# Optimization experiments

Measured on AMD Instinct MI355X. Metric: run time of the kernel, lower is better.

## Reference

```python
import jax, jax.numpy as jnp
import numpy as np

WINDOW = 4  # window_size
H = 8       # n_heads


def setup_inputs() -> dict:
    key = jax.random.key(0)
    ks = jax.random.split(key, 12)
    B, C, T = 4, 512, 1024
    d = C // H
    x = jax.random.normal(ks[0], (B, C, T), dtype=jnp.float32)
    mask = jnp.ones((B, 1, 1, T), dtype=jnp.int32)
    s = 0.02
    Wq = jax.random.normal(ks[1], (C, C), dtype=jnp.float32) * s
    Wk = jax.random.normal(ks[2], (C, C), dtype=jnp.float32) * s
    Wv = jax.random.normal(ks[3], (C, C), dtype=jnp.float32) * s
    Wo = jax.random.normal(ks[4], (C, C), dtype=jnp.float32) * s
    bq = jnp.zeros((C,), jnp.float32)
    bk = jnp.zeros((C,), jnp.float32)
    bv = jnp.zeros((C,), jnp.float32)
    bo = jnp.zeros((C,), jnp.float32)
    rel_std = d ** (-0.5)
    emb_rel_k = jax.random.normal(ks[5], (1, 2 * WINDOW + 1, d), dtype=jnp.float32) * rel_std
    emb_rel_v = jax.random.normal(ks[6], (1, 2 * WINDOW + 1, d), dtype=jnp.float32) * rel_std
    return {"x": x, "mask": mask, "Wq": Wq, "bq": bq, "Wk": Wk, "bk": bk,
            "Wv": Wv, "bv": bv, "Wo": Wo, "bo": bo,
            "emb_rel_k": emb_rel_k, "emb_rel_v": emb_rel_v}


def _slice_rel_emb(emb, T, pad_len, start, end):
    # F.pad(emb, [0,0,pad,pad,0,0]) then [:, start:end] -> [1, 2T-1, d]
    p = jnp.pad(emb, ((0, 0), (pad_len, pad_len), (0, 0)))
    return p[:, start:end]


def reference(x, mask, Wq, bq, Wk, bk, Wv, bv, Wo, bo, emb_rel_k, emb_rel_v):
    B, C, T = x.shape
    d = C // H
    scale = jnp.asarray(np.sqrt(d), x.dtype)

    def proj(Wm, bm):
        return jnp.einsum('oc,bct->bot', Wm, x) + bm[None, :, None]

    def to_heads(t):  # [B,C,T] -> [B,H,T,d]
        return t.reshape(B, H, d, T).transpose(0, 1, 3, 2)

    query = to_heads(proj(Wq, bq))
    key_ = to_heads(proj(Wk, bk))
    value = to_heads(proj(Wv, bv))

    score = jnp.einsum('bhtd,bhsd->bhts', query, key_) / scale

    pad_len = max(0, T - (WINDOW + 1))
    start = max(0, WINDOW + 1 - T)
    end = start + 2 * T - 1

    k_emb = _slice_rel_emb(emb_rel_k, T, pad_len, start, end)  # [1, 2T-1, d]
    rel = jnp.einsum('bhtd,rd->bhtr', query, k_emb[0])          # [B,H,T,2T-1]
    # skew trick: relative -> absolute
    rel = jnp.pad(rel, ((0, 0), (0, 0), (0, 0), (0, 1))).reshape(B, H, 2 * T * T)
    rel = jnp.pad(rel, ((0, 0), (0, 0), (0, T - 1))).reshape(B, H, T + 1, 2 * T - 1)
    score_loc = rel[:, :, :T, T - 1:] / scale
    score = score + score_loc

    score = jnp.where(mask == 0, jnp.asarray(-10000.0, score.dtype), score)
    p_attn = jax.nn.softmax(score, axis=-1)  # dropout=0 (eval)

    output = jnp.einsum('bhts,bhsd->bhtd', p_attn, value)

    # inverse skew: absolute -> relative weights [B,H,T,2T-1]
    pw = jnp.pad(p_attn, ((0, 0), (0, 0), (0, 0), (0, T - 1))).reshape(B, H, T * (2 * T - 1))
    pw = jnp.pad(pw, ((0, 0), (0, 0), (T, 0))).reshape(B, H, T, 2 * T)[:, :, :, 1:]
    v_emb = _slice_rel_emb(emb_rel_v, T, pad_len, start, end)  # [1, 2T-1, d]
    output = output + jnp.einsum('bhtr,rd->bhtd', pw, v_emb[0])

    out = output.transpose(0, 1, 3, 2).reshape(B, C, T)
    return jnp.einsum('oc,bct->bot', Wo, out) + bo[None, :, None]
```

## Files before the change

kernel.cpp:

```cpp
#include <hip/hip_runtime.h>

typedef unsigned short u16;
typedef unsigned int u32;
using f32x4 = __attribute__((ext_vector_type(4))) float;
using s16x8 = __attribute__((ext_vector_type(8))) short;
using u16x4 = __attribute__((ext_vector_type(4))) unsigned short;
using u16x8 = __attribute__((ext_vector_type(8))) unsigned short;

namespace {

constexpr int T = 1024;
constexpr int C = 512;

__device__ inline u16 f2bf(float f) {
  u32 u = __builtin_bit_cast(u32, f);
  u32 r = (u + 0x7fffu + ((u >> 16) & 1u)) >> 16;
  return (u16)r;
}
__device__ inline float bf2f(u16 v) {
  return __builtin_bit_cast(float, (u32)v << 16);
}
__device__ inline f32x4 mfma16(s16x8 a, s16x8 b, f32x4 c) {
  return __builtin_amdgcn_mfma_f32_16x16x32_bf16(a, b, c, 0, 0, 0);
}

__global__ __launch_bounds__(256) void convert_all(
    const float* __restrict__ x, const float* __restrict__ Wq,
    const float* __restrict__ Wk, const float* __restrict__ Wv,
    const float* __restrict__ Wo, u16* __restrict__ xb, u16* __restrict__ Wqb,
    u16* __restrict__ Wkb, u16* __restrict__ Wvb, u16* __restrict__ Wob) {
  const int tid = threadIdx.x;
  const int bid = blockIdx.x;
  const float* src;
  u16* dst;
  size_t off;
  if (bid < 2048) {
    src = x; dst = xb;
    off = ((size_t)bid * 256 + tid) * 4;
  } else {
    const int j = bid - 2048;
    const int w = j >> 8;
    src = w == 0 ? Wq : w == 1 ? Wk : w == 2 ? Wv : Wo;
    dst = w == 0 ? Wqb : w == 1 ? Wkb : w == 2 ? Wvb : Wob;
    off = (((size_t)(j & 255)) * 256 + tid) * 4;
  }
  const float4 v = *reinterpret_cast<const float4*>(src + off);
  u16x4 o;
  o[0] = f2bf(v.x); o[1] = f2bf(v.y); o[2] = f2bf(v.z); o[3] = f2bf(v.w);
  *reinterpret_cast<u16x4*>(dst + off) = o;
}

__global__ __launch_bounds__(256) void qkv_gemm(
    const u16* __restrict__ xb, const u16* __restrict__ Wqb,
    const u16* __restrict__ Wkb, const u16* __restrict__ Wvb,
    const float* __restrict__ bq, const float* __restrict__ bk,
    const float* __restrict__ bv, u16* __restrict__ qb, u16* __restrict__ kb,
    u16* __restrict__ vb) {
  __shared__ u16 Bs[2][128 * 32];
  __shared__ float sbias[64];
  const int tid = threadIdx.x;
  const int z = blockIdx.z;
  const int b = z / 3, wsel = z - 3 * b;
  const u16* W = wsel == 0 ? Wqb : wsel == 1 ? Wkb : Wvb;
  const float* bias = wsel == 0 ? bq : wsel == 1 ? bk : bv;
  const int o0 = blockIdx.y * 64;
  const int t0 = blockIdx.x * 128;
  if (tid < 16)
    *reinterpret_cast<float4*>(&sbias[tid * 4]) =
        *reinterpret_cast<const float4*>(&bias[o0 + tid * 4]);

  const int l = tid & 63, wid = tid >> 6;
  const int wm = wid >> 1, wn = wid & 1;
  const int lr = l & 15, lg = l >> 4;

  const int cpair = tid & 15, tgrp = tid >> 4;
  const u16* xrow =
      xb + ((size_t)(b * C) + 2 * cpair) * T + t0 + 8 * tgrp;

  const u16* Arow0 = W + (size_t)(o0 + 32 * wm + lr) * C + 8 * lg;
  const u16* Arow1 = Arow0 + 16 * C;

  f32x4 acc[2][4] = {};

  auto stage = [&](int kk, int buf) {
    const u16* p = xrow + (size_t)kk * 32 * T;
    const u16x8 v0 = *reinterpret_cast<const u16x8*>(p);
    const u16x8 v1 = *reinterpret_cast<const u16x8*>(p + T);
    char* base = (char*)&Bs[buf][0];
#pragma unroll
    for (int j = 0; j < 8; ++j) {
      const int t = 8 * tgrp + j;
      const u32 w2 = (u32)v0[j] | ((u32)v1[j] << 16);
      *(u32*)(base + ((t * 64 + 4 * cpair) ^ ((t & 3) << 4))) = w2;
    }
  };

  s16x8 a0 = *reinterpret_cast<const s16x8*>(Arow0);
  s16x8 a1 = *reinterpret_cast<const s16x8*>(Arow1);
  stage(0, 0);
  __syncthreads();

  for (int kk = 0; kk < 16; ++kk) {
    s16x8 an0, an1;
    if (kk < 15) {
      an0 = *reinterpret_cast<const s16x8*>(Arow0 + (kk + 1) * 32);
      an1 = *reinterpret_cast<const s16x8*>(Arow1 + (kk + 1) * 32);
      stage(kk + 1, (kk + 1) & 1);
    }
    const char* rb = (const char*)&Bs[kk & 1][0];
#pragma unroll
    for (int nf = 0; nf < 4; ++nf) {
      const int t = 64 * wn + 16 * nf + lr;
      const s16x8 bfrag = *reinterpret_cast<const s16x8*>(
          rb + ((t * 64 + 16 * lg) ^ ((t & 3) << 4)));
      acc[0][nf] = mfma16(a0, bfrag, acc[0][nf]);
      acc[1][nf] = mfma16(a1, bfrag, acc[1][nf]);
    }
    __syncthreads();
    if (kk < 15) { a0 = an0; a1 = an1; }
  }

  const int h = o0 >> 6;
  if (wsel < 2) {
    u16* dst = (wsel == 0) ? qb : kb;
#pragma unroll
    for (int m = 0; m < 2; ++m) {
      const int ob = 32 * wm + 16 * m + 4 * lg;
#pragma unroll
      for (int nf = 0; nf < 4; ++nf) {
        const int t = t0 + 64 * wn + 16 * nf + lr;
        u16x4 pk;
#pragma unroll
        for (int r = 0; r < 4; ++r) pk[r] = f2bf(acc[m][nf][r] + sbias[ob + r]);
        *reinterpret_cast<u16x4*>(
            &dst[((size_t)((b * 8 + h) * T) + t) * 64 + ob]) = pk;
      }
    }
  } else {
#pragma unroll
    for (int m = 0; m < 2; ++m) {
      const int ob = 32 * wm + 16 * m + 4 * lg;
#pragma unroll
      for (int nf = 0; nf < 4; ++nf) {
        const int t = t0 + 64 * wn + 16 * nf + lr;
#pragma unroll
        for (int r = 0; r < 4; ++r)
          vb[((size_t)((b * 8 + h) * 64) + ob + r) * T + t] =
              f2bf(acc[m][nf][r] + sbias[ob + r]);
      }
    }
  }
}

__global__ __launch_bounds__(256) void attn_mfma(
    const u16* __restrict__ qb, const u16* __restrict__ kb,
    const u16* __restrict__ vb, const int* __restrict__ mask,
    const float* __restrict__ ek, const float* __restrict__ ev,
    u16* __restrict__ attb) {
  __shared__ u16 Qs[64 * 64];
  __shared__ u16 Ks[64 * 64];
  __shared__ u16 Vs[64 * 64];
  __shared__ float Ps[4][16 * 68];
  __shared__ float rkk[64][12];
  __shared__ float eks[9][64];
  __shared__ float evs[9][64];
  __shared__ int msk[64];

  const int b = blockIdx.z, h = blockIdx.y, tc = blockIdx.x * 64;
  const int tid = threadIdx.x;
  const int l = tid & 63, wid = tid >> 6;
  const int lr = l & 15, lg = l >> 4;

  const size_t bh = (size_t)(b * 8 + h);
  const u16* qrow = qb + (bh * T + tc) * 64;
  const u16* krow = kb + bh * T * 64;
  const u16* vrow = vb + bh * 64 * T;

  {
    char* qs = (char*)Qs;
#pragma unroll
    for (int rep = 0; rep < 2; ++rep) {
      const int idx = rep * 256 + tid;
      const int t = idx >> 3, slot = idx & 7;
      const u16x8 v =
          *reinterpret_cast<const u16x8*>(&qrow[(size_t)t * 64 + 8 * slot]);
      *(u16x8*)(qs + ((t * 128 + 16 * slot) ^ ((t & 7) << 4))) = v;
    }
  }
  if (tid < 144) {
    reinterpret_cast<float4*>(&eks[0][0])[tid] =
        reinterpret_cast<const float4*>(ek)[tid];
    reinterpret_cast<float4*>(&evs[0][0])[tid] =
        reinterpret_cast<const float4*>(ev)[tid];
  }
  __syncthreads();

  {
    const char* qs = (const char*)Qs;
    for (int task = tid; task < 576; task += 256) {
      const int r = task / 9, w = task - 9 * r;
      float s = 0.f;
      const float* er = &eks[w][0];
#pragma unroll 8
      for (int dd = 0; dd < 64; ++dd) {
        const u16 qv = *(const u16*)(qs + ((r * 128 + 2 * dd) ^ ((r & 7) << 4)));
        s += bf2f(qv) * er[dd];
      }
      rkk[r][w] = 0.125f * s;
    }
  }

  float m[4], lsum[4];
  f32x4 Oa[4] = {};
#pragma unroll
  for (int r = 0; r < 4; ++r) { m[r] = -1e30f; lsum[r] = 0.f; }

  const int tA = 16 * wid + lr;
  s16x8 aq0, aq1;
  {
    const char* qs = (const char*)Qs;
    aq0 = *reinterpret_cast<const s16x8*>(
        qs + ((tA * 128 + 16 * lg) ^ ((tA & 7) << 4)));
    aq1 = *reinterpret_cast<const s16x8*>(
        qs + ((tA * 128 + 16 * (lg + 4)) ^ ((tA & 7) << 4)));
  }

  for (int st = 0; st < 16; ++st) {
    const int s0 = st * 64;
    __syncthreads();
    {
      char* ks_ = (char*)Ks;
      char* vs_ = (char*)Vs;
#pragma unroll
      for (int rep = 0; rep < 2; ++rep) {
        const int idx = rep * 256 + tid;
        const int rrow = idx >> 3, slot = idx & 7;
        const u16x8 kv = *reinterpret_cast<const u16x8*>(
            &krow[(size_t)(s0 + rrow) * 64 + 8 * slot]);
        *(u16x8*)(ks_ + ((rrow * 128 + 16 * slot) ^ ((rrow & 7) << 4))) = kv;
        const u16x8 vv = *reinterpret_cast<const u16x8*>(
            &vrow[(size_t)rrow * T + s0 + 8 * slot]);
        *(u16x8*)(vs_ + ((rrow * 128 + 16 * slot) ^ ((rrow & 7) << 4))) = vv;
      }
      if (tid < 64) msk[tid] = mask[b * T + s0 + tid];
    }
    __syncthreads();

    f32x4 S[4] = {};
    const char* ksb = (const char*)Ks;
#pragma unroll
    for (int nf = 0; nf < 4; ++nf) {
      const int srow = 16 * nf + lr;
      const int swz = (srow & 7) << 4;
      const s16x8 bk0 = *reinterpret_cast<const s16x8*>(
          ksb + ((srow * 128 + 16 * lg) ^ swz));
      S[nf] = mfma16(aq0, bk0, S[nf]);
      const s16x8 bk1 = *reinterpret_cast<const s16x8*>(
          ksb + ((srow * 128 + 16 * (lg + 4)) ^ swz));
      S[nf] = mfma16(aq1, bk1, S[nf]);
    }

    const bool diag = (s0 <= tc + 67) && (s0 + 63 >= tc - 4);

#pragma unroll
    for (int nf = 0; nf < 4; ++nf) {
      const int sl_ = 16 * nf + lr;
      const int mz = msk[sl_];
#pragma unroll
      for (int r = 0; r < 4; ++r) {
        const int tl = 16 * wid + 4 * lg + r;
        float v = S[nf][r] * 0.125f;
        if (diag) {
          const int sd = (s0 + sl_) - (tc + tl);
          if (sd >= -4 && sd <= 4) v += rkk[tl][sd + 4];
        }
        S[nf][r] = (mz == 0) ? -10000.0f : v;
      }
    }

    float pex[4][4], corr[4];
#pragma unroll
    for (int r = 0; r < 4; ++r) {
      float rm = fmaxf(fmaxf(S[0][r], S[1][r]), fmaxf(S[2][r], S[3][r]));
#pragma unroll
      for (int off = 1; off < 16; off <<= 1) rm = fmaxf(rm, __shfl_xor(rm, off));
      const float mn = fmaxf(m[r], rm);
      corr[r] = __expf(m[r] - mn);
      m[r] = mn;
      float rs = 0.f;
#pragma unroll
      for (int nf = 0; nf < 4; ++nf) {
        const float p = __expf(S[nf][r] - mn);
        pex[nf][r] = p;
        rs += p;
      }
#pragma unroll
      for (int off = 1; off < 16; off <<= 1) rs += __shfl_xor(rs, off);
      lsum[r] = lsum[r] * corr[r] + rs;
    }
#pragma unroll
    for (int nf = 0; nf < 4; ++nf) {
      f32x4 o = Oa[nf];
      o[0] *= corr[0]; o[1] *= corr[1]; o[2] *= corr[2]; o[3] *= corr[3];
      Oa[nf] = o;
#pragma unroll
      for (int r = 0; r < 4; ++r)
        Ps[wid][(4 * lg + r) * 68 + 16 * nf + lr] = pex[nf][r];
    }

    const char* vsb = (const char*)Vs;
#pragma unroll
    for (int ks = 0; ks < 2; ++ks) {
      const float* prow = &Ps[wid][lr * 68 + 8 * lg + 32 * ks];
      const float4 p0 = *reinterpret_cast<const float4*>(prow);
      const float4 p1 = *reinterpret_cast<const float4*>(prow + 4);
      s16x8 pa;
      pa[0] = (short)f2bf(p0.x); pa[1] = (short)f2bf(p0.y);
      pa[2] = (short)f2bf(p0.z); pa[3] = (short)f2bf(p0.w);
      pa[4] = (short)f2bf(p1.x); pa[5] = (short)f2bf(p1.y);
      pa[6] = (short)f2bf(p1.z); pa[7] = (short)f2bf(p1.w);
#pragma unroll
      for (int nf = 0; nf < 4; ++nf) {
        const int dd = 16 * nf + lr;
        const s16x8 bv_ = *reinterpret_cast<const s16x8*>(
            vsb + ((dd * 128 + 16 * (lg + 4 * ks)) ^ ((dd & 7) << 4)));
        Oa[nf] = mfma16(pa, bv_, Oa[nf]);
      }
    }

    if (diag) {
#pragma unroll
      for (int r = 0; r < 4; ++r) {
        const int tl = 16 * wid + 4 * lg + r;
        const int tg = tc + tl;
#pragma unroll
        for (int w = 0; w < 9; ++w) {
          const int sl_ = tg - 4 + w - s0;
          if (sl_ >= 0 && sl_ < 64) {
            const float p = Ps[wid][(4 * lg + r) * 68 + sl_];
#pragma unroll
            for (int nf = 0; nf < 4; ++nf)
              Oa[nf][r] += p * evs[w][16 * nf + lr];
          }
        }
      }
    }
  }

#pragma unroll
  for (int nf = 0; nf < 4; ++nf) {
#pragma unroll
    for (int r = 0; r < 4; ++r) {
      const int tl = 16 * wid + 4 * lg + r;
      const float val = Oa[nf][r] / lsum[r];
      attb[(bh * T + tc + tl) * 64 + 16 * nf + lr] = f2bf(val);
    }
  }
}

__global__ __launch_bounds__(256) void out_gemm(
    const u16* __restrict__ Wob, const float* __restrict__ bo,
    const u16* __restrict__ attb, float* __restrict__ out) {
  __shared__ u16 Bs[2][128 * 32];
  __shared__ float sbias[64];
  const int tid = threadIdx.x;
  const int b = blockIdx.z;
  const int o0 = blockIdx.y * 64;
  const int t0 = blockIdx.x * 128;
  if (tid < 16)
    *reinterpret_cast<float4*>(&sbias[tid * 4]) =
        *reinterpret_cast<const float4*>(&bo[o0 + tid * 4]);

  const int l = tid & 63, wid = tid >> 6;
  const int wm = wid >> 1, wn = wid & 1;
  const int lr = l & 15, lg = l >> 4;

  const int slot = tid & 3, trow = tid >> 2;
  const u16* Arow0 = Wob + (size_t)(o0 + 32 * wm + lr) * C + 8 * lg;
  const u16* Arow1 = Arow0 + 16 * C;

  f32x4 acc[2][4] = {};

  auto stage = [&](int kk, int buf) {
    const int c0 = kk * 32;
    const int h = c0 >> 6, dd0 = c0 & 63;
    char* base = (char*)&Bs[buf][0];
#pragma unroll
    for (int rep = 0; rep < 2; ++rep) {
      const int t = rep * 64 + trow;
      const u16x8 v = *reinterpret_cast<const u16x8*>(
          &attb[((size_t)((b * 8 + h) * T) + t0 + t) * 64 + dd0 + 8 * slot]);
      *(u16x8*)(base + ((t * 64 + 16 * slot) ^ ((t & 3) << 4))) = v;
    }
  };

  s16x8 a0 = *reinterpret_cast<const s16x8*>(Arow0);
  s16x8 a1 = *reinterpret_cast<const s16x8*>(Arow1);
  stage(0, 0);
  __syncthreads();

  for (int kk = 0; kk < 16; ++kk) {
    s16x8 an0, an1;
    if (kk < 15) {
      an0 = *reinterpret_cast<const s16x8*>(Arow0 + (kk + 1) * 32);
      an1 = *reinterpret_cast<const s16x8*>(Arow1 + (kk + 1) * 32);
      stage(kk + 1, (kk + 1) & 1);
    }
    const char* rb = (const char*)&Bs[kk & 1][0];
#pragma unroll
    for (int nf = 0; nf < 4; ++nf) {
      const int t = 64 * wn + 16 * nf + lr;
      const s16x8 bfrag = *reinterpret_cast<const s16x8*>(
          rb + ((t * 64 + 16 * lg) ^ ((t & 3) << 4)));
      acc[0][nf] = mfma16(a0, bfrag, acc[0][nf]);
      acc[1][nf] = mfma16(a1, bfrag, acc[1][nf]);
    }
    __syncthreads();
    if (kk < 15) { a0 = an0; a1 = an1; }
  }

#pragma unroll
  for (int m = 0; m < 2; ++m) {
    const int ol = 32 * wm + 16 * m + 4 * lg;
#pragma unroll
    for (int nf = 0; nf < 4; ++nf) {
      const int t = t0 + 64 * wn + 16 * nf + lr;
#pragma unroll
      for (int r = 0; r < 4; ++r)
        out[((size_t)(b * C) + o0 + ol + r) * T + t] =
            acc[m][nf][r] + sbias[ol + r];
    }
  }
}

}

extern "C" void kernel_launch(void* const* d_in, const int* in_sizes, int n_in,
                              void* d_out, int out_size, void* d_ws,
                              size_t ws_size, hipStream_t stream) {
  const float* x    = (const float*)d_in[0];
  const int*   mask = (const int*)d_in[1];
  const float* Wq   = (const float*)d_in[2];
  const float* bq   = (const float*)d_in[3];
  const float* Wk   = (const float*)d_in[4];
  const float* bk   = (const float*)d_in[5];
  const float* Wv   = (const float*)d_in[6];
  const float* bv   = (const float*)d_in[7];
  const float* Wo   = (const float*)d_in[8];
  const float* bo   = (const float*)d_in[9];
  const float* ek   = (const float*)d_in[10];
  const float* ev   = (const float*)d_in[11];
  float* out = (float*)d_out;

  char* ws = (char*)d_ws;
  u16* xb   = (u16*)(ws);
  u16* Wqb  = (u16*)(ws + 4194304);
  u16* Wkb  = (u16*)(ws + 4718592);
  u16* Wvb  = (u16*)(ws + 5242880);
  u16* Wob  = (u16*)(ws + 5767168);
  u16* qb   = (u16*)(ws + 6291456);
  u16* kb   = (u16*)(ws + 10485760);
  u16* vb   = (u16*)(ws + 14680064);
  u16* attb = (u16*)(ws + 18874368);

  convert_all<<<dim3(3072), dim3(256), 0, stream>>>(x, Wq, Wk, Wv, Wo, xb, Wqb,
                                                    Wkb, Wvb, Wob);
  qkv_gemm<<<dim3(8, 8, 12), dim3(256), 0, stream>>>(xb, Wqb, Wkb, Wvb, bq, bk,
                                                     bv, qb, kb, vb);
  attn_mfma<<<dim3(16, 8, 4), dim3(256), 0, stream>>>(qb, kb, vb, mask, ek, ev,
                                                      attb);
  out_gemm<<<dim3(8, 8, 4), dim3(256), 0, stream>>>(Wob, bo, attb, out);
}
```

Measured before the change: 99.71 us.

## Load K/V fragments directly from global into registers, drop LDS staging and barriers

```diff
diff --git a/kernel.cpp b/kernel.cpp
--- a/kernel.cpp
+++ b/kernel.cpp
@@ -158,13 +158,11 @@
     const float* __restrict__ ek, const float* __restrict__ ev,
     u16* __restrict__ attb) {
   __shared__ u16 Qs[64 * 64];
-  __shared__ u16 Ks[64 * 64];
-  __shared__ u16 Vs[64 * 64];
   __shared__ float Ps[4][16 * 68];
   __shared__ float rkk[64][12];
   __shared__ float eks[9][64];
   __shared__ float evs[9][64];
-  __shared__ int msk[64];
+  __shared__ int msk[1024];
 
   const int b = blockIdx.z, h = blockIdx.y, tc = blockIdx.x * 64;
   const int tid = threadIdx.x;
@@ -173,8 +171,8 @@
 
   const size_t bh = (size_t)(b * 8 + h);
   const u16* qrow = qb + (bh * T + tc) * 64;
-  const u16* krow = kb + bh * T * 64;
-  const u16* vrow = vb + bh * 64 * T;
+  const u16* kbh = kb + bh * T * 64;
+  const u16* vbh = vb + bh * 64 * T;
 
   {
     char* qs = (char*)Qs;
@@ -193,6 +191,8 @@
     reinterpret_cast<float4*>(&evs[0][0])[tid] =
         reinterpret_cast<const float4*>(ev)[tid];
   }
+  reinterpret_cast<int4*>(msk)[tid] =
+      reinterpret_cast<const int4*>(mask + b * T)[tid];
   __syncthreads();
 
   {
@@ -224,40 +224,31 @@
     aq1 = *reinterpret_cast<const s16x8*>(
         qs + ((tA * 128 + 16 * (lg + 4)) ^ ((tA & 7) << 4)));
   }
+  __syncthreads();
 
   for (int st = 0; st < 16; ++st) {
     const int s0 = st * 64;
-    __syncthreads();
-    {
-      char* ks_ = (char*)Ks;
-      char* vs_ = (char*)Vs;
-#pragma unroll
-      for (int rep = 0; rep < 2; ++rep) {
-        const int idx = rep * 256 + tid;
-        const int rrow = idx >> 3, slot = idx & 7;
-        const u16x8 kv = *reinterpret_cast<const u16x8*>(
-            &krow[(size_t)(s0 + rrow) * 64 + 8 * slot]);
-        *(u16x8*)(ks_ + ((rrow * 128 + 16 * slot) ^ ((rrow & 7) << 4))) = kv;
-        const u16x8 vv = *reinterpret_cast<const u16x8*>(
-            &vrow[(size_t)rrow * T + s0 + 8 * slot]);
-        *(u16x8*)(vs_ + ((rrow * 128 + 16 * slot) ^ ((rrow & 7) << 4))) = vv;
-      }
-      if (tid < 64) msk[tid] = mask[b * T + s0 + tid];
-    }
-    __syncthreads();
-
+
+    s16x8 bk0[4], bk1[4];
+#pragma unroll
+    for (int nf = 0; nf < 4; ++nf) {
+      const u16* kr = kbh + (size_t)(s0 + 16 * nf + lr) * 64;
+      bk0[nf] = *reinterpret_cast<const s16x8*>(kr + 8 * lg);
+      bk1[nf] = *reinterpret_cast<const s16x8*>(kr + 32 + 8 * lg);
+    }
     f32x4 S[4] = {};
-    const char* ksb = (const char*)Ks;
-#pragma unroll
-    for (int nf = 0; nf < 4; ++nf) {
-      const int srow = 16 * nf + lr;
-      const int swz = (srow & 7) << 4;
-      const s16x8 bk0 = *reinterpret_cast<const s16x8*>(
-          ksb + ((srow * 128 + 16 * lg) ^ swz));
-      S[nf] = mfma16(aq0, bk0, S[nf]);
-      const s16x8 bk1 = *reinterpret_cast<const s16x8*>(
-          ksb + ((srow * 128 + 16 * (lg + 4)) ^ swz));
-      S[nf] = mfma16(aq1, bk1, S[nf]);
+#pragma unroll
+    for (int nf = 0; nf < 4; ++nf) {
+      S[nf] = mfma16(aq0, bk0[nf], S[nf]);
+      S[nf] = mfma16(aq1, bk1[nf], S[nf]);
+    }
+
+    s16x8 bv0[4], bv1[4];
+#pragma unroll
+    for (int nf = 0; nf < 4; ++nf) {
+      const u16* vr = vbh + (size_t)(16 * nf + lr) * T + s0 + 8 * lg;
+      bv0[nf] = *reinterpret_cast<const s16x8*>(vr);
+      bv1[nf] = *reinterpret_cast<const s16x8*>(vr + 32);
     }
 
     const bool diag = (s0 <= tc + 67) && (s0 + 63 >= tc - 4);
@@ -265,7 +256,7 @@
 #pragma unroll
     for (int nf = 0; nf < 4; ++nf) {
       const int sl_ = 16 * nf + lr;
-      const int mz = msk[sl_];
+      const int mz = msk[s0 + sl_];
 #pragma unroll
       for (int r = 0; r < 4; ++r) {
         const int tl = 16 * wid + 4 * lg + r;
@@ -308,7 +299,6 @@
         Ps[wid][(4 * lg + r) * 68 + 16 * nf + lr] = pex[nf][r];
     }
 
-    const char* vsb = (const char*)Vs;
 #pragma unroll
     for (int ks = 0; ks < 2; ++ks) {
       const float* prow = &Ps[wid][lr * 68 + 8 * lg + 32 * ks];
@@ -320,12 +310,8 @@
       pa[4] = (short)f2bf(p1.x); pa[5] = (short)f2bf(p1.y);
       pa[6] = (short)f2bf(p1.z); pa[7] = (short)f2bf(p1.w);
 #pragma unroll
-      for (int nf = 0; nf < 4; ++nf) {
-        const int dd = 16 * nf + lr;
-        const s16x8 bv_ = *reinterpret_cast<const s16x8*>(
-            vsb + ((dd * 128 + 16 * (lg + 4 * ks)) ^ ((dd & 7) << 4)));
-        Oa[nf] = mfma16(pa, bv_, Oa[nf]);
-      }
+      for (int nf = 0; nf < 4; ++nf)
+        Oa[nf] = mfma16(pa, ks == 0 ? bv0[nf] : bv1[nf], Oa[nf]);
     }
 
     if (diag) {
```

New measurement: 118.7 us. +19.0%, slower.

## Split attention over two key halves and merge with a combine kernel

Applied to the files above, without the earlier changes.

```diff
diff --git a/kernel.cpp b/kernel.cpp
--- a/kernel.cpp
+++ b/kernel.cpp
@@ -152,32 +152,34 @@
   }
 }
 
-__global__ __launch_bounds__(256) void attn_mfma(
+__global__ __launch_bounds__(256) void attn_split(
     const u16* __restrict__ qb, const u16* __restrict__ kb,
     const u16* __restrict__ vb, const int* __restrict__ mask,
     const float* __restrict__ ek, const float* __restrict__ ev,
-    u16* __restrict__ attb) {
-  __shared__ u16 Qs[64 * 64];
+    u16* __restrict__ op0, u16* __restrict__ op1, float2* __restrict__ mlb) {
   __shared__ u16 Ks[64 * 64];
   __shared__ u16 Vs[64 * 64];
-  __shared__ float Ps[4][16 * 68];
+  __shared__ u16 PsQ[4][16 * 72];
   __shared__ float rkk[64][12];
   __shared__ float eks[9][64];
   __shared__ float evs[9][64];
-  __shared__ int msk[64];
-
-  const int b = blockIdx.z, h = blockIdx.y, tc = blockIdx.x * 64;
+  __shared__ int msk[512];
+
+  const int z = blockIdx.z;
+  const int b = z >> 1, shalf = z & 1;
+  const int h = blockIdx.y, tc = blockIdx.x * 64;
   const int tid = threadIdx.x;
   const int l = tid & 63, wid = tid >> 6;
   const int lr = l & 15, lg = l >> 4;
+  const int sbase = shalf * 512;
 
   const size_t bh = (size_t)(b * 8 + h);
   const u16* qrow = qb + (bh * T + tc) * 64;
-  const u16* krow = kb + bh * T * 64;
-  const u16* vrow = vb + bh * 64 * T;
+  const u16* kbh = kb + bh * T * 64;
+  const u16* vbh = vb + bh * 64 * T;
 
   {
-    char* qs = (char*)Qs;
+    char* qs = (char*)&PsQ[0][0];
 #pragma unroll
     for (int rep = 0; rep < 2; ++rep) {
       const int idx = rep * 256 + tid;
@@ -193,10 +195,13 @@
     reinterpret_cast<float4*>(&evs[0][0])[tid] =
         reinterpret_cast<const float4*>(ev)[tid];
   }
+  if (tid < 128)
+    reinterpret_cast<int4*>(msk)[tid] =
+        reinterpret_cast<const int4*>(mask + b * T + sbase)[tid];
   __syncthreads();
 
   {
-    const char* qs = (const char*)Qs;
+    const char* qs = (const char*)&PsQ[0][0];
     for (int task = tid; task < 576; task += 256) {
       const int r = task / 9, w = task - 9 * r;
       float s = 0.f;
@@ -218,14 +223,15 @@
   const int tA = 16 * wid + lr;
   s16x8 aq0, aq1;
   {
-    const char* qs = (const char*)Qs;
+    const char* qs = (const char*)&PsQ[0][0];
     aq0 = *reinterpret_cast<const s16x8*>(
         qs + ((tA * 128 + 16 * lg) ^ ((tA & 7) << 4)));
     aq1 = *reinterpret_cast<const s16x8*>(
         qs + ((tA * 128 + 16 * (lg + 4)) ^ ((tA & 7) << 4)));
   }
-
-  for (int st = 0; st < 16; ++st) {
+  __syncthreads();
+
+  for (int st = shalf * 8; st < shalf * 8 + 8; ++st) {
     const int s0 = st * 64;
     __syncthreads();
     {
@@ -236,13 +242,12 @@
         const int idx = rep * 256 + tid;
         const int rrow = idx >> 3, slot = idx & 7;
         const u16x8 kv = *reinterpret_cast<const u16x8*>(
-            &krow[(size_t)(s0 + rrow) * 64 + 8 * slot]);
+            &kbh[(size_t)(s0 + rrow) * 64 + 8 * slot]);
         *(u16x8*)(ks_ + ((rrow * 128 + 16 * slot) ^ ((rrow & 7) << 4))) = kv;
         const u16x8 vv = *reinterpret_cast<const u16x8*>(
-            &vrow[(size_t)rrow * T + s0 + 8 * slot]);
+            &vbh[(size_t)rrow * T + s0 + 8 * slot]);
         *(u16x8*)(vs_ + ((rrow * 128 + 16 * slot) ^ ((rrow & 7) << 4))) = vv;
       }
-      if (tid < 64) msk[tid] = mask[b * T + s0 + tid];
     }
     __syncthreads();
 
@@ -265,7 +270,7 @@
 #pragma unroll
     for (int nf = 0; nf < 4; ++nf) {
       const int sl_ = 16 * nf + lr;
-      const int mz = msk[sl_];
+      const int mz = msk[s0 - sbase + sl_];
 #pragma unroll
       for (int r = 0; r < 4; ++r) {
         const int tl = 16 * wid + 4 * lg + r;
@@ -305,20 +310,14 @@
       Oa[nf] = o;
 #pragma unroll
       for (int r = 0; r < 4; ++r)
-        Ps[wid][(4 * lg + r) * 68 + 16 * nf + lr] = pex[nf][r];
+        PsQ[wid][(4 * lg + r) * 72 + 16 * nf + lr] = f2bf(pex[nf][r]);
     }
 
     const char* vsb = (const char*)Vs;
 #pragma unroll
     for (int ks = 0; ks < 2; ++ks) {
-      const float* prow = &Ps[wid][lr * 68 + 8 * lg + 32 * ks];
-      const float4 p0 = *reinterpret_cast<const float4*>(prow);
-      const float4 p1 = *reinterpret_cast<const float4*>(prow + 4);
-      s16x8 pa;
-      pa[0] = (short)f2bf(p0.x); pa[1] = (short)f2bf(p0.y);
-      pa[2] = (short)f2bf(p0.z); pa[3] = (short)f2bf(p0.w);
-      pa[4] = (short)f2bf(p1.x); pa[5] = (short)f2bf(p1.y);
-      pa[6] = (short)f2bf(p1.z); pa[7] = (short)f2bf(p1.w);
+      const s16x8 pa = *reinterpret_cast<const s16x8*>(
+          &PsQ[wid][lr * 72 + 8 * lg + 32 * ks]);
 #pragma unroll
       for (int nf = 0; nf < 4; ++nf) {
         const int dd = 16 * nf + lr;
@@ -337,7 +336,7 @@
         for (int w = 0; w < 9; ++w) {
           const int sl_ = tg - 4 + w - s0;
           if (sl_ >= 0 && sl_ < 64) {
-            const float p = Ps[wid][(4 * lg + r) * 68 + sl_];
+            const float p = bf2f(PsQ[wid][(4 * lg + r) * 72 + sl_]);
 #pragma unroll
             for (int nf = 0; nf < 4; ++nf)
               Oa[nf][r] += p * evs[w][16 * nf + lr];
@@ -347,15 +346,44 @@
     }
   }
 
-#pragma unroll
-  for (int nf = 0; nf < 4; ++nf) {
+  u16* op = shalf ? op1 : op0;
+#pragma unroll
+  for (int nf = 0; nf < 4; ++nf)
 #pragma unroll
     for (int r = 0; r < 4; ++r) {
       const int tl = 16 * wid + 4 * lg + r;
-      const float val = Oa[nf][r] / lsum[r];
-      attb[(bh * T + tc + tl) * 64 + 16 * nf + lr] = f2bf(val);
-    }
-  }
+      op[(bh * T + tc + tl) * 64 + 16 * nf + lr] = f2bf(Oa[nf][r]);
+    }
+  if (lr == 0) {
+#pragma unroll
+    for (int r = 0; r < 4; ++r) {
+      const int tl = 16 * wid + 4 * lg + r;
+      float2 v;
+      v.x = m[r];
+      v.y = lsum[r];
+      mlb[(size_t)shalf * 32768 + bh * T + tc + tl] = v;
+    }
+  }
+}
+
+__global__ __launch_bounds__(256) void merge_halves(
+    const u16* __restrict__ op0, const u16* __restrict__ op1,
+    const float2* __restrict__ mlb, u16* __restrict__ attb) {
+  const int tid = threadIdx.x;
+  const int row = blockIdx.x * 16 + (tid >> 4);
+  const int dd = (tid & 15) * 4;
+  const float2 ml0 = mlb[row];
+  const float2 ml1 = mlb[32768 + row];
+  const float mm = fmaxf(ml0.x, ml1.x);
+  const float a0 = __expf(ml0.x - mm), a1 = __expf(ml1.x - mm);
+  const float inv = 1.0f / (a0 * ml0.y + a1 * ml1.y);
+  const u16x4 v0 = *reinterpret_cast<const u16x4*>(&op0[(size_t)row * 64 + dd]);
+  const u16x4 v1 = *reinterpret_cast<const u16x4*>(&op1[(size_t)row * 64 + dd]);
+  u16x4 o;
+#pragma unroll
+  for (int j = 0; j < 4; ++j)
+    o[j] = f2bf((bf2f(v0[j]) * a0 + bf2f(v1[j]) * a1) * inv);
+  *reinterpret_cast<u16x4*>(&attb[(size_t)row * 64 + dd]) = o;
 }
 
 __global__ __launch_bounds__(256) void out_gemm(
@@ -462,12 +490,16 @@
   u16* kb   = (u16*)(ws + 10485760);
   u16* vb   = (u16*)(ws + 14680064);
   u16* attb = (u16*)(ws + 18874368);
+  u16* op0  = xb;
+  u16* op1  = (u16*)(ws + 23068672);
+  float2* mlb = (float2*)(ws + 27262976);
 
   convert_all<<<dim3(3072), dim3(256), 0, stream>>>(x, Wq, Wk, Wv, Wo, xb, Wqb,
                                                     Wkb, Wvb, Wob);
   qkv_gemm<<<dim3(8, 8, 12), dim3(256), 0, stream>>>(xb, Wqb, Wkb, Wvb, bq, bk,
                                                      bv, qb, kb, vb);
-  attn_mfma<<<dim3(16, 8, 4), dim3(256), 0, stream>>>(qb, kb, vb, mask, ek, ev,
-                                                      attb);
+  attn_split<<<dim3(16, 8, 8), dim3(256), 0, stream>>>(qb, kb, vb, mask, ek, ev,
+                                                       op0, op1, mlb);
+  merge_halves<<<dim3(2048), dim3(256), 0, stream>>>(op0, op1, mlb, attb);
   out_gemm<<<dim3(8, 8, 4), dim3(256), 0, stream>>>(Wob, bo, attb, out);
 }
```

Result: slower. 116.6 us (+16.9%).
